# Kernel optimization log

Hardware: AMD Instinct MI355X
Metric: run time of the kernel (lower is better)

Reference implementation:

```python
import jax, jax.numpy as jnp
import numpy as np

N_NODES = 20000
N_EDGES = 320000
N_FEAT = 128
MLP_HID = 64
N_GRAPHS = 16
N_LAYERS = 5
EPS = 1e-5


def setup_inputs() -> dict:
    key = jax.random.key(0)
    ks = jax.random.split(key, 8)
    x = jax.random.normal(ks[0], (N_NODES, N_FEAT), dtype=jnp.float32)
    edge_index = jax.random.randint(ks[1], (2, N_EDGES), 0, N_NODES, dtype=jnp.int64)
    batch = jnp.sort(jax.random.randint(ks[2], (N_NODES,), 0, N_GRAPHS, dtype=jnp.int64))
    W1 = jax.random.normal(ks[3], (N_LAYERS, N_FEAT, MLP_HID), dtype=jnp.float32) * 0.05
    b1 = jnp.zeros((N_LAYERS, MLP_HID), dtype=jnp.float32)
    W2 = jax.random.normal(ks[4], (N_LAYERS, MLP_HID, N_FEAT), dtype=jnp.float32) * 0.05
    b2 = jnp.zeros((N_LAYERS, N_FEAT), dtype=jnp.float32)
    gn_weight = jnp.ones((N_LAYERS, N_FEAT), dtype=jnp.float32)
    gn_bias = jnp.zeros((N_LAYERS, N_FEAT), dtype=jnp.float32)
    gn_scale = jnp.ones((N_LAYERS, N_FEAT), dtype=jnp.float32)
    lin_w = jax.random.normal(ks[5], (N_FEAT, 1), dtype=jnp.float32) * 0.05
    lin_b = jnp.zeros((1,), dtype=jnp.float32)
    return {"x": x, "edge_index": edge_index, "batch": batch,
            "W1": W1, "b1": b1, "W2": W2, "b2": b2,
            "gn_weight": gn_weight, "gn_bias": gn_bias, "gn_scale": gn_scale,
            "lin_w": lin_w, "lin_b": lin_b}


def _conv(h, src, dst, W1, b1, W2, b2):
    # message MLP is per-source-node, so compute MLP(x) once per node,
    # then gather by src and scatter-add to dst. Self loops add m[i] at i.
    m = jax.nn.relu(h @ W1 + b1) @ W2 + b2  # [N, C]
    return jax.ops.segment_sum(m[src], dst, num_segments=N_NODES) + m


def _graph_norm(h, batch, cnt, w, b, a):
    mean = jax.ops.segment_sum(h, batch, num_segments=N_GRAPHS) / cnt  # [G, C]
    out = h - a * mean[batch]
    var = jax.ops.segment_sum(out * out, batch, num_segments=N_GRAPHS) / cnt
    out = out * jax.lax.rsqrt(var[batch] + EPS)
    return w * out + b


def reference(x, edge_index, batch, W1, b1, W2, b2, gn_weight, gn_bias, gn_scale, lin_w, lin_b):
    src, dst = edge_index[0], edge_index[1]
    cnt = jax.ops.segment_sum(jnp.ones((N_NODES, 1), x.dtype), batch,
                              num_segments=N_GRAPHS)
    cnt = jnp.maximum(cnt, 1.0)  # [G, 1]
    h = x
    for i in range(N_LAYERS):
        g = _conv(h, src, dst, W1[i], b1[i], W2[i], b2[i])
        g = _graph_norm(g, batch, cnt, gn_weight[i], gn_bias[i], gn_scale[i])
        g = jax.nn.relu(g)  # dropout is identity in eval mode
        h = g if i == 0 else g + h  # residual from layer 2 onward
    pooled = jax.ops.segment_sum(h, batch, num_segments=N_GRAPHS) / cnt  # [G, C]
    return pooled @ lin_w + lin_b  # [G, 1]
```

## Files before the change

kernel.cpp:

```cpp
#include <hip/hip_runtime.h>

#define N_NODES 20000
#define N_EDGES 320000
#define N_FEAT 128
#define MLP_HID 64
#define N_GRAPHS 16
#define N_LAYERS 5
#define EPS 1e-5f

typedef __attribute__((ext_vector_type(8))) short short8;
typedef __attribute__((ext_vector_type(4))) float f32x4;

__device__ inline float bf2f(unsigned short u) { return __uint_as_float(((unsigned)u) << 16); }
__device__ inline unsigned short f2bf(float f) {
  unsigned u = __float_as_uint(f);
  u += 0x7FFF + ((u >> 16) & 1);
  return (unsigned short)(u >> 16);
}


__global__ __launch_bounds__(256) void k_deg(const int* __restrict__ dst, int* __restrict__ deg) {
  int e = blockIdx.x * 256 + threadIdx.x;
  atomicAdd(&deg[dst[e]], 1);
}

__global__ __launch_bounds__(1024) void k_scan(const int* __restrict__ deg, int* __restrict__ rowptr,
                                               int* __restrict__ cursor, const int* __restrict__ batch,
                                               float* __restrict__ cntf, float* __restrict__ zero_region) {
  __shared__ int sdata[1024];
  __shared__ int spos[17];
  constexpr int CH = 20;
  int t = threadIdx.x;
  for (int i = t; i < 22528; i += 1024) zero_region[i] = 0.0f;
  int base = t * CH;
  int loc[CH];
  int partial = 0;
#pragma unroll
  for (int i = 0; i < CH; i++) {
    int idx = base + i;
    int v = (idx < N_NODES) ? deg[idx] : 0;
    loc[i] = v;
    partial += v;
  }
  sdata[t] = partial;
  __syncthreads();
  for (int off = 1; off < 1024; off <<= 1) {
    int v = (t >= off) ? sdata[t - off] : 0;
    __syncthreads();
    sdata[t] += v;
    __syncthreads();
  }
  int run = sdata[t] - partial;
#pragma unroll
  for (int i = 0; i < CH; i++) {
    int idx = base + i;
    if (idx < N_NODES) {
      rowptr[idx] = run;
      cursor[idx] = run;
      run += loc[i];
    }
  }
  if (t == 1023) rowptr[N_NODES] = sdata[1023];
  if (t < 17) {
    int lo = 0, hi = N_NODES;
    while (lo < hi) {
      int mid = (lo + hi) >> 1;
      if (batch[mid] < t) lo = mid + 1; else hi = mid;
    }
    spos[t] = lo;
  }
  __syncthreads();
  if (t < N_GRAPHS) cntf[t] = fmaxf((float)(spos[t + 1] - spos[t]), 1.0f);
}

__global__ __launch_bounds__(256) void k_fill(const int* __restrict__ src, const int* __restrict__ dst,
                                              int* __restrict__ cursor, int* __restrict__ src_sorted) {
  int e = blockIdx.x * 256 + threadIdx.x;
  int d = dst[e];
  int p = atomicAdd(&cursor[d], 1);
  src_sorted[p] = src[e];
}


__global__ __launch_bounds__(256) void k_prep(const float* __restrict__ W1, const float* __restrict__ W2,
                                              unsigned short* __restrict__ w1t, unsigned short* __restrict__ w2t) {
  int idx = blockIdx.x * 256 + threadIdx.x;
  if (idx < 40960) {
    int l = idx >> 13, rem = idx & 8191;
    int n = rem >> 7, k = rem & 127;
    w1t[idx] = f2bf(W1[l * 8192 + k * 64 + n]);
  } else {
    int j = idx - 40960;
    int l = j >> 13, rem = j & 8191;
    int n = rem >> 6, k = rem & 63;
    w2t[j] = f2bf(W2[l * 8192 + k * 128 + n]);
  }
}


#define PADK 136
#define PADH 72

__global__ __launch_bounds__(256) void k_mlpA(const float* __restrict__ xin, const float* __restrict__ gin,
                                              float* __restrict__ h, unsigned short* __restrict__ mout,
                                              const unsigned short* __restrict__ w1t,
                                              const unsigned short* __restrict__ w2t,
                                              const float* __restrict__ b1, const float* __restrict__ b2,
                                              const int* __restrict__ batch,
                                              const float* __restrict__ s1, const float* __restrict__ s2,
                                              const float* __restrict__ cntf,
                                              const float* __restrict__ gw, const float* __restrict__ gb,
                                              const float* __restrict__ ga, int mode) {
  __shared__ __align__(16) short hS[64 * PADK];
  __shared__ __align__(16) short w1S[64 * PADK];
  __shared__ __align__(16) short hidS[64 * PADH];
  __shared__ __align__(16) short w2S[128 * PADH];
  __shared__ float b1S[64];
  __shared__ float b2S[128];
  int t = threadIdx.x;
  int r0 = blockIdx.x * 64;
#pragma unroll
  for (int i = 0; i < 8; i++) {
    int idx = t + i * 256;
    int row = idx >> 5, c4 = idx & 31;
    int grow = r0 + row;
    float4 v = make_float4(0.f, 0.f, 0.f, 0.f);
    if (grow < N_NODES) {
      if (mode == 0) {
        v = ((const float4*)xin)[(size_t)grow * 32 + c4];
      } else {
        int gg = batch[grow];
        float invc = 1.0f / cntf[gg];
        float4 sm = ((const float4*)s1)[gg * 32 + c4];
        float4 se = ((const float4*)s2)[gg * 32 + c4];
        float4 av = ((const float4*)ga)[c4];
        float4 wv = ((const float4*)gw)[c4];
        float4 bv = ((const float4*)gb)[c4];
        float4 gv = ((const float4*)gin)[(size_t)grow * 32 + c4];
        float4 hv = make_float4(0.f, 0.f, 0.f, 0.f);
        if (mode == 2) hv = ((const float4*)h)[(size_t)grow * 32 + c4];
#define APPLY1(X)                                                         \
        {                                                                 \
          float mean = sm.X * invc;                                       \
          float ex2 = se.X * invc;                                        \
          float ac = av.X;                                                \
          float var = fmaxf(ex2 - mean * mean * (2.0f * ac - ac * ac), 0.0f); \
          float d = gv.X - ac * mean;                                     \
          float y = wv.X * (d * rsqrtf(var + EPS)) + bv.X;                \
          y = fmaxf(y, 0.0f);                                             \
          v.X = y + hv.X;                                                 \
        }
        APPLY1(x) APPLY1(y) APPLY1(z) APPLY1(w)
#undef APPLY1
        ((float4*)h)[(size_t)grow * 32 + c4] = v;
      }
    }
    ushort4 s;
    s.x = f2bf(v.x); s.y = f2bf(v.y); s.z = f2bf(v.z); s.w = f2bf(v.w);
    *(ushort4*)&hS[row * PADK + c4 * 4] = s;
  }
#pragma unroll
  for (int i = 0; i < 4; i++) {
    int idx = t + i * 256;
    *(int4*)&w1S[(idx >> 4) * PADK + (idx & 15) * 8] = ((const int4*)w1t)[idx];
    *(int4*)&w2S[(idx >> 3) * PADH + (idx & 7) * 8] = ((const int4*)w2t)[idx];
  }
  if (t < 64) b1S[t] = b1[t];
  else if (t < 192) b2S[t - 64] = b2[t - 64];
  __syncthreads();

  int w = t >> 6, lane = t & 63, lm = lane & 15, quad = lane >> 4;
  int mrow = w * 16 + lm;
  int orow = w * 16 + quad * 4;

  f32x4 zero = {0.f, 0.f, 0.f, 0.f};
  f32x4 acc[4] = {zero, zero, zero, zero};
#pragma unroll
  for (int k0 = 0; k0 < 128; k0 += 32) {
    short8 a = *(const short8*)&hS[mrow * PADK + k0 + quad * 8];
#pragma unroll
    for (int nt = 0; nt < 4; nt++) {
      short8 b = *(const short8*)&w1S[(nt * 16 + lm) * PADK + k0 + quad * 8];
      acc[nt] = __builtin_amdgcn_mfma_f32_16x16x32_bf16(a, b, acc[nt], 0, 0, 0);
    }
  }
#pragma unroll
  for (int nt = 0; nt < 4; nt++) {
    int col = nt * 16 + lm;
    float bb = b1S[col];
#pragma unroll
    for (int r = 0; r < 4; r++)
      hidS[(orow + r) * PADH + col] = (short)f2bf(fmaxf(acc[nt][r] + bb, 0.0f));
  }
  __syncthreads();

  f32x4 acc2[8] = {zero, zero, zero, zero, zero, zero, zero, zero};
#pragma unroll
  for (int k0 = 0; k0 < 64; k0 += 32) {
    short8 a = *(const short8*)&hidS[mrow * PADH + k0 + quad * 8];
#pragma unroll
    for (int nt = 0; nt < 8; nt++) {
      short8 b = *(const short8*)&w2S[(nt * 16 + lm) * PADH + k0 + quad * 8];
      acc2[nt] = __builtin_amdgcn_mfma_f32_16x16x32_bf16(a, b, acc2[nt], 0, 0, 0);
    }
  }
#pragma unroll
  for (int nt = 0; nt < 8; nt++) {
    int col = nt * 16 + lm;
    float bb = b2S[col];
#pragma unroll
    for (int r = 0; r < 4; r++)
      hS[(orow + r) * PADK + col] = (short)f2bf(acc2[nt][r] + bb);
  }
  __syncthreads();
#pragma unroll
  for (int i = 0; i < 4; i++) {
    int idx = t + i * 256;
    int row = idx >> 4, cc = idx & 15;
    if (r0 + row < N_NODES)
      ((int4*)mout)[(size_t)(r0 + row) * 16 + cc] = *(const int4*)&hS[row * PADK + cc * 8];
  }
}


__global__ __launch_bounds__(256) void k_scatter(const unsigned short* __restrict__ mbf, float* __restrict__ g,
                                                 const int* __restrict__ rowptr, const int* __restrict__ srcs) {
  int node = (blockIdx.x * 256 + threadIdx.x) >> 6;
  int lane = threadIdx.x & 63;
  int quarter = lane >> 4;
  int q16 = lane & 15;
  const float4* m4 = (const float4*)mbf;
  float acc[8];
  union BU { float4 f; unsigned short u[8]; };
  if (quarter == 0) {
    BU U; U.f = m4[(size_t)node * 16 + q16];
#pragma unroll
    for (int j = 0; j < 8; j++) acc[j] = bf2f(U.u[j]);
  } else {
#pragma unroll
    for (int j = 0; j < 8; j++) acc[j] = 0.0f;
  }
  int e = rowptr[node], e1 = rowptr[node + 1];
  for (; e + 16 <= e1; e += 16) {
    int i0 = srcs[e + quarter];
    int i1 = srcs[e + 4 + quarter];
    int i2 = srcs[e + 8 + quarter];
    int i3 = srcs[e + 12 + quarter];
    BU U0, U1, U2, U3;
    U0.f = m4[(size_t)i0 * 16 + q16];
    U1.f = m4[(size_t)i1 * 16 + q16];
    U2.f = m4[(size_t)i2 * 16 + q16];
    U3.f = m4[(size_t)i3 * 16 + q16];
#pragma unroll
    for (int j = 0; j < 8; j++)
      acc[j] += (bf2f(U0.u[j]) + bf2f(U1.u[j])) + (bf2f(U2.u[j]) + bf2f(U3.u[j]));
  }
  for (; e + 4 <= e1; e += 4) {
    BU U0; U0.f = m4[(size_t)srcs[e + quarter] * 16 + q16];
#pragma unroll
    for (int j = 0; j < 8; j++) acc[j] += bf2f(U0.u[j]);
  }
  if (e + quarter < e1) {
    BU U0; U0.f = m4[(size_t)srcs[e + quarter] * 16 + q16];
#pragma unroll
    for (int j = 0; j < 8; j++) acc[j] += bf2f(U0.u[j]);
  }
#pragma unroll
  for (int j = 0; j < 8; j++) {
    acc[j] += __shfl_xor(acc[j], 16);
    acc[j] += __shfl_xor(acc[j], 32);
  }
  if (quarter == 0) {
    float4* g4 = (float4*)(g + (size_t)node * 128 + q16 * 8);
    g4[0] = make_float4(acc[0], acc[1], acc[2], acc[3]);
    g4[1] = make_float4(acc[4], acc[5], acc[6], acc[7]);
  }
}


#define STAT_CHUNK 8

__global__ __launch_bounds__(128) void k_stats(const float* __restrict__ in, const int* __restrict__ batch,
                                               float* __restrict__ s1, float* __restrict__ s2) {
  int n0 = blockIdx.x * STAT_CHUNK;
  int c = threadIdx.x;
  int curg = batch[n0];
  float a1 = 0.0f, a2 = 0.0f;
#pragma unroll
  for (int k = 0; k < STAT_CHUNK; k++) {
    int n = n0 + k;
    int gg = batch[n];
    if (gg != curg) {
      atomicAdd(&s1[curg * 128 + c], a1);
      atomicAdd(&s2[curg * 128 + c], a2);
      a1 = 0.0f; a2 = 0.0f;
      curg = gg;
    }
    float v = in[(size_t)n * 128 + c];
    a1 += v;
    a2 += v * v;
  }
  atomicAdd(&s1[curg * 128 + c], a1);
  atomicAdd(&s2[curg * 128 + c], a2);
}


__global__ __launch_bounds__(256) void k_applyPool(const float* __restrict__ gin, const float* __restrict__ h,
                                                   const int* __restrict__ batch,
                                                   const float* __restrict__ s1, const float* __restrict__ s2,
                                                   const float* __restrict__ cntf,
                                                   const float* __restrict__ gw, const float* __restrict__ gb,
                                                   const float* __restrict__ ga, float* __restrict__ pooled) {
  __shared__ float poolL[128];
  int t = threadIdx.x;
  if (t < 128) poolL[t] = 0.0f;
  __syncthreads();
  int idx = blockIdx.x * 256 + t;
  int n = idx >> 5, c4 = idx & 31;
  int g0 = batch[blockIdx.x * 8];
  int gg = batch[n];
  float invc = 1.0f / cntf[gg];
  float4 sm = ((const float4*)s1)[gg * 32 + c4];
  float4 se = ((const float4*)s2)[gg * 32 + c4];
  float4 av = ((const float4*)ga)[c4];
  float4 wv = ((const float4*)gw)[c4];
  float4 bv = ((const float4*)gb)[c4];
  float4 gv = ((const float4*)gin)[idx];
  float4 hv = ((const float4*)h)[idx];
  float4 o;
#define APPLY1(X)                                                          \
  {                                                                        \
    float mean = sm.X * invc;                                              \
    float ex2 = se.X * invc;                                               \
    float ac = av.X;                                                       \
    float var = fmaxf(ex2 - mean * mean * (2.0f * ac - ac * ac), 0.0f);    \
    float d = gv.X - ac * mean;                                            \
    float y = wv.X * (d * rsqrtf(var + EPS)) + bv.X;                       \
    o.X = fmaxf(y, 0.0f) + hv.X;                                           \
  }
  APPLY1(x) APPLY1(y) APPLY1(z) APPLY1(w)
#undef APPLY1
  if (gg == g0) {
    atomicAdd(&poolL[c4 * 4 + 0], o.x);
    atomicAdd(&poolL[c4 * 4 + 1], o.y);
    atomicAdd(&poolL[c4 * 4 + 2], o.z);
    atomicAdd(&poolL[c4 * 4 + 3], o.w);
  } else {
    atomicAdd(&pooled[gg * 128 + c4 * 4 + 0], o.x);
    atomicAdd(&pooled[gg * 128 + c4 * 4 + 1], o.y);
    atomicAdd(&pooled[gg * 128 + c4 * 4 + 2], o.z);
    atomicAdd(&pooled[gg * 128 + c4 * 4 + 3], o.w);
  }
  __syncthreads();
  if (t < 128) atomicAdd(&pooled[g0 * 128 + t], poolL[t]);
}


__global__ __launch_bounds__(256) void k_final(const float* __restrict__ pooled, const float* __restrict__ cntf,
                                               const float* __restrict__ lw, const float* __restrict__ lb,
                                               float* __restrict__ out) {
  int lane = threadIdx.x & 63, wave = threadIdx.x >> 6;
  for (int gi = 0; gi < 4; gi++) {
    int gidx = wave * 4 + gi;
    float s = pooled[gidx * 128 + lane] * lw[lane] + pooled[gidx * 128 + 64 + lane] * lw[64 + lane];
    for (int o = 32; o >= 1; o >>= 1) s += __shfl_down(s, o);
    if (lane == 0) out[gidx] = s / cntf[gidx] + lb[0];
  }
}


extern "C" void kernel_launch(void* const* d_in, const int* in_sizes, int n_in,
                              void* d_out, int out_size, void* d_ws, size_t ws_size,
                              hipStream_t stream) {
  const float* x = (const float*)d_in[0];
  const int* ei = (const int*)d_in[1];
  const int* batch = (const int*)d_in[2];
  const float* W1 = (const float*)d_in[3];
  const float* b1 = (const float*)d_in[4];
  const float* W2 = (const float*)d_in[5];
  const float* b2 = (const float*)d_in[6];
  const float* gnw = (const float*)d_in[7];
  const float* gnb = (const float*)d_in[8];
  const float* gna = (const float*)d_in[9];
  const float* lw = (const float*)d_in[10];
  const float* lb = (const float*)d_in[11];
  float* out = (float*)d_out;

  const int* srcI = ei;
  const int* dstI = ei + N_EDGES;

  char* p = (char*)d_ws;
  float* hbuf = (float*)(p + 0);
  unsigned short* mbuf = (unsigned short*)(p + 10240000);
  float* gbuf = (float*)(p + 15360000);
  int* src_sorted = (int*)(p + 25600000);
  int* rowptr = (int*)(p + 26880000);
  int* cursor = (int*)(p + 26960128);
  int* deg = (int*)(p + 27040256);
  float* cntf = (float*)(p + 27120384);
  unsigned short* w1t = (unsigned short*)(p + 27120512);
  unsigned short* w2t = (unsigned short*)(p + 27202432);
  float* sbufs = (float*)(p + 27284352);
  float* pooled = (float*)(p + 27366272);

  hipMemsetAsync(deg, 0, N_NODES * sizeof(int), stream);
  k_deg<<<N_EDGES / 256, 256, 0, stream>>>(dstI, deg);
  k_scan<<<1, 1024, 0, stream>>>(deg, rowptr, cursor, batch, cntf, sbufs);
  k_fill<<<N_EDGES / 256, 256, 0, stream>>>(srcI, dstI, cursor, src_sorted);
  k_prep<<<320, 256, 0, stream>>>(W1, W2, w1t, w2t);

  for (int i = 0; i < N_LAYERS; i++) {
    int pi = (i > 0) ? (i - 1) : 0;
    int mode = (i == 0) ? 0 : (i == 1 ? 1 : 2);
    k_mlpA<<<(N_NODES + 63) / 64, 256, 0, stream>>>(
        x, gbuf, hbuf, mbuf, w1t + (size_t)i * 8192, w2t + (size_t)i * 8192,
        b1 + (size_t)i * 64, b2 + (size_t)i * 128,
        batch, sbufs + (size_t)pi * 4096, sbufs + (size_t)pi * 4096 + 2048, cntf,
        gnw + (size_t)pi * 128, gnb + (size_t)pi * 128, gna + (size_t)pi * 128, mode);
    k_scatter<<<N_NODES / 4, 256, 0, stream>>>(mbuf, gbuf, rowptr, src_sorted);
    k_stats<<<N_NODES / STAT_CHUNK, 128, 0, stream>>>(gbuf, batch,
                                                      sbufs + (size_t)i * 4096, sbufs + (size_t)i * 4096 + 2048);
  }

  k_applyPool<<<N_NODES * N_FEAT / 4 / 256, 256, 0, stream>>>(
      gbuf, hbuf, batch, sbufs + 4 * 4096, sbufs + 4 * 4096 + 2048, cntf,
      gnw + 4 * 128, gnb + 4 * 128, gna + 4 * 128, pooled);
  k_final<<<1, 256, 0, stream>>>(pooled, cntf, lw, lb, out);
}
```

Before: 349.4 us.

## Fuse per-layer kernels into one cooperative persistent kernel with grid syncs

Replaces the per-layer sequence of MLP, gather-scatter, stats, apply-pool and final kernels with a single cooperative kernel. The kernel loops over layers, runs each stage as a grid-stride loop over tiles or tasks, and separates stages with grid.sync(). This removes about 17 kernel launches and their launch gaps. In exchange the grid is capped by occupancy, which limits parallelism in the memory-bound gather stage. Grid-wide barriers add their own cost, and the tile loop reloads the weights into shared memory for every tile.

```diff
diff --git a/kernel.cpp b/kernel.cpp
--- a/kernel.cpp
+++ b/kernel.cpp
@@ -1,4 +1,7 @@
 #include <hip/hip_runtime.h>
+#include <hip/hip_cooperative_groups.h>
+
+namespace cg = cooperative_groups;
 
 #define N_NODES 20000
 #define N_EDGES 320000
@@ -80,7 +83,6 @@
   int p = atomicAdd(&cursor[d], 1);
   src_sorted[p] = src[e];
 }
-
 
 __global__ __launch_bounds__(256) void k_prep(const float* __restrict__ W1, const float* __restrict__ W2,
                                               unsigned short* __restrict__ w1t, unsigned short* __restrict__ w2t) {
@@ -100,271 +102,302 @@
 
 #define PADK 136
 #define PADH 72
-
-__global__ __launch_bounds__(256) void k_mlpA(const float* __restrict__ xin, const float* __restrict__ gin,
-                                              float* __restrict__ h, unsigned short* __restrict__ mout,
-                                              const unsigned short* __restrict__ w1t,
-                                              const unsigned short* __restrict__ w2t,
-                                              const float* __restrict__ b1, const float* __restrict__ b2,
-                                              const int* __restrict__ batch,
-                                              const float* __restrict__ s1, const float* __restrict__ s2,
-                                              const float* __restrict__ cntf,
-                                              const float* __restrict__ gw, const float* __restrict__ gb,
-                                              const float* __restrict__ ga, int mode) {
-  __shared__ __align__(16) short hS[64 * PADK];
-  __shared__ __align__(16) short w1S[64 * PADK];
-  __shared__ __align__(16) short hidS[64 * PADH];
-  __shared__ __align__(16) short w2S[128 * PADH];
-  __shared__ float b1S[64];
-  __shared__ float b2S[128];
+#define SMEM_BYTES 63232
+
+__global__ __launch_bounds__(256, 2) void k_mega(
+    const float* __restrict__ x, const int* __restrict__ batch,
+    const float* __restrict__ b1g, const float* __restrict__ b2g,
+    const float* __restrict__ gnw, const float* __restrict__ gnb, const float* __restrict__ gna,
+    const float* __restrict__ lw, const float* __restrict__ lb,
+    float* __restrict__ h, unsigned short* __restrict__ m, float* __restrict__ g,
+    const int* __restrict__ rowptr, const int* __restrict__ srcs,
+    const float* __restrict__ cntf, const unsigned short* __restrict__ w1t,
+    const unsigned short* __restrict__ w2t,
+    float* __restrict__ sbufs, float* __restrict__ pooled, float* __restrict__ out) {
+  cg::grid_group grid = cg::this_grid();
+  __shared__ __align__(16) char smem[SMEM_BYTES];
+  short* hS = (short*)(smem);
+  short* w1S = (short*)(smem + 17408);
+  short* hidS = (short*)(smem + 34816);
+  short* w2S = (short*)(smem + 44032);
+  float* b1S = (float*)(smem + 62464);
+  float* b2S = (float*)(smem + 62720);
   int t = threadIdx.x;
-  int r0 = blockIdx.x * 64;
-#pragma unroll
-  for (int i = 0; i < 8; i++) {
-    int idx = t + i * 256;
-    int row = idx >> 5, c4 = idx & 31;
-    int grow = r0 + row;
-    float4 v = make_float4(0.f, 0.f, 0.f, 0.f);
-    if (grow < N_NODES) {
-      if (mode == 0) {
-        v = ((const float4*)xin)[(size_t)grow * 32 + c4];
+
+  for (int layer = 0; layer < N_LAYERS; layer++) {
+    const unsigned short* w1 = w1t + (size_t)layer * 8192;
+    const unsigned short* w2 = w2t + (size_t)layer * 8192;
+    const float* b1 = b1g + (size_t)layer * 64;
+    const float* b2 = b2g + (size_t)layer * 128;
+    int pi = (layer > 0) ? (layer - 1) : 0;
+    const float* s1 = sbufs + (size_t)pi * 4096;
+    const float* s2 = s1 + 2048;
+    const float* gw = gnw + (size_t)pi * 128;
+    const float* gb = gnb + (size_t)pi * 128;
+    const float* ga = gna + (size_t)pi * 128;
+    int mode = (layer == 0) ? 0 : (layer == 1 ? 1 : 2);
+
+    for (int tile = blockIdx.x; tile < 313; tile += gridDim.x) {
+      int r0 = tile * 64;
+#pragma unroll
+      for (int i = 0; i < 8; i++) {
+        int idx = t + i * 256;
+        int row = idx >> 5, c4 = idx & 31;
+        int grow = r0 + row;
+        float4 v = make_float4(0.f, 0.f, 0.f, 0.f);
+        if (grow < N_NODES) {
+          if (mode == 0) {
+            v = ((const float4*)x)[(size_t)grow * 32 + c4];
+          } else {
+            int gg = batch[grow];
+            float invc = 1.0f / cntf[gg];
+            float4 sm = ((const float4*)s1)[gg * 32 + c4];
+            float4 se = ((const float4*)s2)[gg * 32 + c4];
+            float4 av = ((const float4*)ga)[c4];
+            float4 wv = ((const float4*)gw)[c4];
+            float4 bv = ((const float4*)gb)[c4];
+            float4 gv = ((const float4*)g)[(size_t)grow * 32 + c4];
+            float4 hv = make_float4(0.f, 0.f, 0.f, 0.f);
+            if (mode == 2) hv = ((const float4*)h)[(size_t)grow * 32 + c4];
+#define APPLY1(X)                                                         \
+            {                                                             \
+              float mean = sm.X * invc;                                   \
+              float ex2 = se.X * invc;                                    \
+              float ac = av.X;                                            \
+              float var = fmaxf(ex2 - mean * mean * (2.0f * ac - ac * ac), 0.0f); \
+              float d = gv.X - ac * mean;                                 \
+              float y = wv.X * (d * rsqrtf(var + EPS)) + bv.X;            \
+              y = fmaxf(y, 0.0f);                                         \
+              v.X = y + hv.X;                                             \
+            }
+            APPLY1(x) APPLY1(y) APPLY1(z) APPLY1(w)
+#undef APPLY1
+            ((float4*)h)[(size_t)grow * 32 + c4] = v;
+          }
+        }
+        ushort4 s;
+        s.x = f2bf(v.x); s.y = f2bf(v.y); s.z = f2bf(v.z); s.w = f2bf(v.w);
+        *(ushort4*)&hS[row * PADK + c4 * 4] = s;
+      }
+#pragma unroll
+      for (int i = 0; i < 4; i++) {
+        int idx = t + i * 256;
+        *(int4*)&w1S[(idx >> 4) * PADK + (idx & 15) * 8] = ((const int4*)w1)[idx];
+        *(int4*)&w2S[(idx >> 3) * PADH + (idx & 7) * 8] = ((const int4*)w2)[idx];
+      }
+      if (t < 64) b1S[t] = b1[t];
+      else if (t < 192) b2S[t - 64] = b2[t - 64];
+      __syncthreads();
+
+      int w = t >> 6, lane = t & 63, lm = lane & 15, quad = lane >> 4;
+      int mrow = w * 16 + lm;
+      int orow = w * 16 + quad * 4;
+
+      f32x4 zero = {0.f, 0.f, 0.f, 0.f};
+      f32x4 acc[4] = {zero, zero, zero, zero};
+#pragma unroll
+      for (int k0 = 0; k0 < 128; k0 += 32) {
+        short8 a = *(const short8*)&hS[mrow * PADK + k0 + quad * 8];
+#pragma unroll
+        for (int nt = 0; nt < 4; nt++) {
+          short8 b = *(const short8*)&w1S[(nt * 16 + lm) * PADK + k0 + quad * 8];
+          acc[nt] = __builtin_amdgcn_mfma_f32_16x16x32_bf16(a, b, acc[nt], 0, 0, 0);
+        }
+      }
+#pragma unroll
+      for (int nt = 0; nt < 4; nt++) {
+        int col = nt * 16 + lm;
+        float bb = b1S[col];
+#pragma unroll
+        for (int r = 0; r < 4; r++)
+          hidS[(orow + r) * PADH + col] = (short)f2bf(fmaxf(acc[nt][r] + bb, 0.0f));
+      }
+      __syncthreads();
+
+      f32x4 acc2[8] = {zero, zero, zero, zero, zero, zero, zero, zero};
+#pragma unroll
+      for (int k0 = 0; k0 < 64; k0 += 32) {
+        short8 a = *(const short8*)&hidS[mrow * PADH + k0 + quad * 8];
+#pragma unroll
+        for (int nt = 0; nt < 8; nt++) {
+          short8 b = *(const short8*)&w2S[(nt * 16 + lm) * PADH + k0 + quad * 8];
+          acc2[nt] = __builtin_amdgcn_mfma_f32_16x16x32_bf16(a, b, acc2[nt], 0, 0, 0);
+        }
+      }
+#pragma unroll
+      for (int nt = 0; nt < 8; nt++) {
+        int col = nt * 16 + lm;
+        float bb = b2S[col];
+#pragma unroll
+        for (int r = 0; r < 4; r++)
+          hS[(orow + r) * PADK + col] = (short)f2bf(acc2[nt][r] + bb);
+      }
+      __syncthreads();
+#pragma unroll
+      for (int i = 0; i < 4; i++) {
+        int idx = t + i * 256;
+        int row = idx >> 4, cc = idx & 15;
+        if (r0 + row < N_NODES)
+          ((int4*)m)[(size_t)(r0 + row) * 16 + cc] = *(const int4*)&hS[row * PADK + cc * 8];
+      }
+      __syncthreads();
+    }
+    grid.sync();
+
+    {
+      int lane = t & 63;
+      int quarter = lane >> 4;
+      int q16 = lane & 15;
+      const float4* m4 = (const float4*)m;
+      for (int task = blockIdx.x; task < 5000; task += gridDim.x) {
+        int node = task * 4 + (t >> 6);
+        float acc[8];
+        union BU { float4 f; unsigned short u[8]; };
+        if (quarter == 0) {
+          BU U; U.f = m4[(size_t)node * 16 + q16];
+#pragma unroll
+          for (int j = 0; j < 8; j++) acc[j] = bf2f(U.u[j]);
+        } else {
+#pragma unroll
+          for (int j = 0; j < 8; j++) acc[j] = 0.0f;
+        }
+        int e = rowptr[node], e1 = rowptr[node + 1];
+        for (; e + 16 <= e1; e += 16) {
+          int i0 = srcs[e + quarter];
+          int i1 = srcs[e + 4 + quarter];
+          int i2 = srcs[e + 8 + quarter];
+          int i3 = srcs[e + 12 + quarter];
+          BU U0, U1, U2, U3;
+          U0.f = m4[(size_t)i0 * 16 + q16];
+          U1.f = m4[(size_t)i1 * 16 + q16];
+          U2.f = m4[(size_t)i2 * 16 + q16];
+          U3.f = m4[(size_t)i3 * 16 + q16];
+#pragma unroll
+          for (int j = 0; j < 8; j++)
+            acc[j] += (bf2f(U0.u[j]) + bf2f(U1.u[j])) + (bf2f(U2.u[j]) + bf2f(U3.u[j]));
+        }
+        for (; e + 4 <= e1; e += 4) {
+          BU U0; U0.f = m4[(size_t)srcs[e + quarter] * 16 + q16];
+#pragma unroll
+          for (int j = 0; j < 8; j++) acc[j] += bf2f(U0.u[j]);
+        }
+        if (e + quarter < e1) {
+          BU U0; U0.f = m4[(size_t)srcs[e + quarter] * 16 + q16];
+#pragma unroll
+          for (int j = 0; j < 8; j++) acc[j] += bf2f(U0.u[j]);
+        }
+#pragma unroll
+        for (int j = 0; j < 8; j++) {
+          acc[j] += __shfl_xor(acc[j], 16);
+          acc[j] += __shfl_xor(acc[j], 32);
+        }
+        if (quarter == 0) {
+          float4* g4 = (float4*)(g + (size_t)node * 128 + q16 * 8);
+          g4[0] = make_float4(acc[0], acc[1], acc[2], acc[3]);
+          g4[1] = make_float4(acc[4], acc[5], acc[6], acc[7]);
+        }
+      }
+    }
+    grid.sync();
+
+    {
+      float* s1w = sbufs + (size_t)layer * 4096;
+      float* s2w = s1w + 2048;
+      int half = t >> 7, c = t & 127;
+      for (int task = blockIdx.x; task < 1250; task += gridDim.x) {
+        int n0 = task * 16 + half * 8;
+        int curg = batch[n0];
+        float a1 = 0.0f, a2 = 0.0f;
+#pragma unroll
+        for (int k = 0; k < 8; k++) {
+          int n = n0 + k;
+          int gg = batch[n];
+          if (gg != curg) {
+            atomicAdd(&s1w[curg * 128 + c], a1);
+            atomicAdd(&s2w[curg * 128 + c], a2);
+            a1 = 0.0f; a2 = 0.0f;
+            curg = gg;
+          }
+          float v = g[(size_t)n * 128 + c];
+          a1 += v;
+          a2 += v * v;
+        }
+        atomicAdd(&s1w[curg * 128 + c], a1);
+        atomicAdd(&s2w[curg * 128 + c], a2);
+      }
+    }
+    grid.sync();
+  }
+
+  {
+    const float* s1 = sbufs + 4 * 4096;
+    const float* s2 = s1 + 2048;
+    const float* gw = gnw + 4 * 128;
+    const float* gb = gnb + 4 * 128;
+    const float* ga = gna + 4 * 128;
+    float4* poolT = (float4*)smem;
+    int c4 = t & 31;
+    for (int task = blockIdx.x; task < 2500; task += gridDim.x) {
+      int idx = task * 256 + t;
+      int n = idx >> 5;
+      int gg = batch[n];
+      float invc = 1.0f / cntf[gg];
+      float4 sm = ((const float4*)s1)[gg * 32 + c4];
+      float4 se = ((const float4*)s2)[gg * 32 + c4];
+      float4 av = ((const float4*)ga)[c4];
+      float4 wv = ((const float4*)gw)[c4];
+      float4 bv = ((const float4*)gb)[c4];
+      float4 gv = ((const float4*)g)[idx];
+      float4 hv = ((const float4*)h)[idx];
+      float4 o;
+#define APPLY1(X)                                                          \
+      {                                                                    \
+        float mean = sm.X * invc;                                          \
+        float ex2 = se.X * invc;                                           \
+        float ac = av.X;                                                   \
+        float var = fmaxf(ex2 - mean * mean * (2.0f * ac - ac * ac), 0.0f);\
+        float d = gv.X - ac * mean;                                        \
+        float y = wv.X * (d * rsqrtf(var + EPS)) + bv.X;                   \
+        o.X = fmaxf(y, 0.0f) + hv.X;                                       \
+      }
+      APPLY1(x) APPLY1(y) APPLY1(z) APPLY1(w)
+#undef APPLY1
+      poolT[t] = o;
+      __syncthreads();
+      int n0 = task * 8;
+      if (batch[n0] == batch[n0 + 7]) {
+        if (t < 32) {
+          float4 s = poolT[t];
+#pragma unroll
+          for (int r = 1; r < 8; r++) {
+            float4 v = poolT[r * 32 + t];
+            s.x += v.x; s.y += v.y; s.z += v.z; s.w += v.w;
+          }
+          int gt = batch[n0];
+          atomicAdd(&pooled[gt * 128 + t * 4 + 0], s.x);
+          atomicAdd(&pooled[gt * 128 + t * 4 + 1], s.y);
+          atomicAdd(&pooled[gt * 128 + t * 4 + 2], s.z);
+          atomicAdd(&pooled[gt * 128 + t * 4 + 3], s.w);
+        }
       } else {
-        int gg = batch[grow];
-        float invc = 1.0f / cntf[gg];
-        float4 sm = ((const float4*)s1)[gg * 32 + c4];
-        float4 se = ((const float4*)s2)[gg * 32 + c4];
-        float4 av = ((const float4*)ga)[c4];
-        float4 wv = ((const float4*)gw)[c4];
-        float4 bv = ((const float4*)gb)[c4];
-        float4 gv = ((const float4*)gin)[(size_t)grow * 32 + c4];
-        float4 hv = make_float4(0.f, 0.f, 0.f, 0.f);
-        if (mode == 2) hv = ((const float4*)h)[(size_t)grow * 32 + c4];
-#define APPLY1(X)                                                         \
-        {                                                                 \
-          float mean = sm.X * invc;                                       \
-          float ex2 = se.X * invc;                                        \
-          float ac = av.X;                                                \
-          float var = fmaxf(ex2 - mean * mean * (2.0f * ac - ac * ac), 0.0f); \
-          float d = gv.X - ac * mean;                                     \
-          float y = wv.X * (d * rsqrtf(var + EPS)) + bv.X;                \
-          y = fmaxf(y, 0.0f);                                             \
-          v.X = y + hv.X;                                                 \
-        }
-        APPLY1(x) APPLY1(y) APPLY1(z) APPLY1(w)
-#undef APPLY1
-        ((float4*)h)[(size_t)grow * 32 + c4] = v;
-      }
-    }
-    ushort4 s;
-    s.x = f2bf(v.x); s.y = f2bf(v.y); s.z = f2bf(v.z); s.w = f2bf(v.w);
-    *(ushort4*)&hS[row * PADK + c4 * 4] = s;
-  }
-#pragma unroll
-  for (int i = 0; i < 4; i++) {
-    int idx = t + i * 256;
-    *(int4*)&w1S[(idx >> 4) * PADK + (idx & 15) * 8] = ((const int4*)w1t)[idx];
-    *(int4*)&w2S[(idx >> 3) * PADH + (idx & 7) * 8] = ((const int4*)w2t)[idx];
-  }
-  if (t < 64) b1S[t] = b1[t];
-  else if (t < 192) b2S[t - 64] = b2[t - 64];
-  __syncthreads();
-
-  int w = t >> 6, lane = t & 63, lm = lane & 15, quad = lane >> 4;
-  int mrow = w * 16 + lm;
-  int orow = w * 16 + quad * 4;
-
-  f32x4 zero = {0.f, 0.f, 0.f, 0.f};
-  f32x4 acc[4] = {zero, zero, zero, zero};
-#pragma unroll
-  for (int k0 = 0; k0 < 128; k0 += 32) {
-    short8 a = *(const short8*)&hS[mrow * PADK + k0 + quad * 8];
-#pragma unroll
-    for (int nt = 0; nt < 4; nt++) {
-      short8 b = *(const short8*)&w1S[(nt * 16 + lm) * PADK + k0 + quad * 8];
-      acc[nt] = __builtin_amdgcn_mfma_f32_16x16x32_bf16(a, b, acc[nt], 0, 0, 0);
-    }
-  }
-#pragma unroll
-  for (int nt = 0; nt < 4; nt++) {
-    int col = nt * 16 + lm;
-    float bb = b1S[col];
-#pragma unroll
-    for (int r = 0; r < 4; r++)
-      hidS[(orow + r) * PADH + col] = (short)f2bf(fmaxf(acc[nt][r] + bb, 0.0f));
-  }
-  __syncthreads();
-
-  f32x4 acc2[8] = {zero, zero, zero, zero, zero, zero, zero, zero};
-#pragma unroll
-  for (int k0 = 0; k0 < 64; k0 += 32) {
-    short8 a = *(const short8*)&hidS[mrow * PADH + k0 + quad * 8];
-#pragma unroll
-    for (int nt = 0; nt < 8; nt++) {
-      short8 b = *(const short8*)&w2S[(nt * 16 + lm) * PADH + k0 + quad * 8];
-      acc2[nt] = __builtin_amdgcn_mfma_f32_16x16x32_bf16(a, b, acc2[nt], 0, 0, 0);
-    }
-  }
-#pragma unroll
-  for (int nt = 0; nt < 8; nt++) {
-    int col = nt * 16 + lm;
-    float bb = b2S[col];
-#pragma unroll
-    for (int r = 0; r < 4; r++)
-      hS[(orow + r) * PADK + col] = (short)f2bf(acc2[nt][r] + bb);
-  }
-  __syncthreads();
-#pragma unroll
-  for (int i = 0; i < 4; i++) {
-    int idx = t + i * 256;
-    int row = idx >> 4, cc = idx & 15;
-    if (r0 + row < N_NODES)
-      ((int4*)mout)[(size_t)(r0 + row) * 16 + cc] = *(const int4*)&hS[row * PADK + cc * 8];
-  }
-}
-
-
-__global__ __launch_bounds__(256) void k_scatter(const unsigned short* __restrict__ mbf, float* __restrict__ g,
-                                                 const int* __restrict__ rowptr, const int* __restrict__ srcs) {
-  int node = (blockIdx.x * 256 + threadIdx.x) >> 6;
-  int lane = threadIdx.x & 63;
-  int quarter = lane >> 4;
-  int q16 = lane & 15;
-  const float4* m4 = (const float4*)mbf;
-  float acc[8];
-  union BU { float4 f; unsigned short u[8]; };
-  if (quarter == 0) {
-    BU U; U.f = m4[(size_t)node * 16 + q16];
-#pragma unroll
-    for (int j = 0; j < 8; j++) acc[j] = bf2f(U.u[j]);
-  } else {
-#pragma unroll
-    for (int j = 0; j < 8; j++) acc[j] = 0.0f;
-  }
-  int e = rowptr[node], e1 = rowptr[node + 1];
-  for (; e + 16 <= e1; e += 16) {
-    int i0 = srcs[e + quarter];
-    int i1 = srcs[e + 4 + quarter];
-    int i2 = srcs[e + 8 + quarter];
-    int i3 = srcs[e + 12 + quarter];
-    BU U0, U1, U2, U3;
-    U0.f = m4[(size_t)i0 * 16 + q16];
-    U1.f = m4[(size_t)i1 * 16 + q16];
-    U2.f = m4[(size_t)i2 * 16 + q16];
-    U3.f = m4[(size_t)i3 * 16 + q16];
-#pragma unroll
-    for (int j = 0; j < 8; j++)
-      acc[j] += (bf2f(U0.u[j]) + bf2f(U1.u[j])) + (bf2f(U2.u[j]) + bf2f(U3.u[j]));
-  }
-  for (; e + 4 <= e1; e += 4) {
-    BU U0; U0.f = m4[(size_t)srcs[e + quarter] * 16 + q16];
-#pragma unroll
-    for (int j = 0; j < 8; j++) acc[j] += bf2f(U0.u[j]);
-  }
-  if (e + quarter < e1) {
-    BU U0; U0.f = m4[(size_t)srcs[e + quarter] * 16 + q16];
-#pragma unroll
-    for (int j = 0; j < 8; j++) acc[j] += bf2f(U0.u[j]);
-  }
-#pragma unroll
-  for (int j = 0; j < 8; j++) {
-    acc[j] += __shfl_xor(acc[j], 16);
-    acc[j] += __shfl_xor(acc[j], 32);
-  }
-  if (quarter == 0) {
-    float4* g4 = (float4*)(g + (size_t)node * 128 + q16 * 8);
-    g4[0] = make_float4(acc[0], acc[1], acc[2], acc[3]);
-    g4[1] = make_float4(acc[4], acc[5], acc[6], acc[7]);
-  }
-}
-
-
-#define STAT_CHUNK 8
-
-__global__ __launch_bounds__(128) void k_stats(const float* __restrict__ in, const int* __restrict__ batch,
-                                               float* __restrict__ s1, float* __restrict__ s2) {
-  int n0 = blockIdx.x * STAT_CHUNK;
-  int c = threadIdx.x;
-  int curg = batch[n0];
-  float a1 = 0.0f, a2 = 0.0f;
-#pragma unroll
-  for (int k = 0; k < STAT_CHUNK; k++) {
-    int n = n0 + k;
-    int gg = batch[n];
-    if (gg != curg) {
-      atomicAdd(&s1[curg * 128 + c], a1);
-      atomicAdd(&s2[curg * 128 + c], a2);
-      a1 = 0.0f; a2 = 0.0f;
-      curg = gg;
-    }
-    float v = in[(size_t)n * 128 + c];
-    a1 += v;
-    a2 += v * v;
-  }
-  atomicAdd(&s1[curg * 128 + c], a1);
-  atomicAdd(&s2[curg * 128 + c], a2);
-}
-
-
-__global__ __launch_bounds__(256) void k_applyPool(const float* __restrict__ gin, const float* __restrict__ h,
-                                                   const int* __restrict__ batch,
-                                                   const float* __restrict__ s1, const float* __restrict__ s2,
-                                                   const float* __restrict__ cntf,
-                                                   const float* __restrict__ gw, const float* __restrict__ gb,
-                                                   const float* __restrict__ ga, float* __restrict__ pooled) {
-  __shared__ float poolL[128];
-  int t = threadIdx.x;
-  if (t < 128) poolL[t] = 0.0f;
-  __syncthreads();
-  int idx = blockIdx.x * 256 + t;
-  int n = idx >> 5, c4 = idx & 31;
-  int g0 = batch[blockIdx.x * 8];
-  int gg = batch[n];
-  float invc = 1.0f / cntf[gg];
-  float4 sm = ((const float4*)s1)[gg * 32 + c4];
-  float4 se = ((const float4*)s2)[gg * 32 + c4];
-  float4 av = ((const float4*)ga)[c4];
-  float4 wv = ((const float4*)gw)[c4];
-  float4 bv = ((const float4*)gb)[c4];
-  float4 gv = ((const float4*)gin)[idx];
-  float4 hv = ((const float4*)h)[idx];
-  float4 o;
-#define APPLY1(X)                                                          \
-  {                                                                        \
-    float mean = sm.X * invc;                                              \
-    float ex2 = se.X * invc;                                               \
-    float ac = av.X;                                                       \
-    float var = fmaxf(ex2 - mean * mean * (2.0f * ac - ac * ac), 0.0f);    \
-    float d = gv.X - ac * mean;                                            \
-    float y = wv.X * (d * rsqrtf(var + EPS)) + bv.X;                       \
-    o.X = fmaxf(y, 0.0f) + hv.X;                                           \
-  }
-  APPLY1(x) APPLY1(y) APPLY1(z) APPLY1(w)
-#undef APPLY1
-  if (gg == g0) {
-    atomicAdd(&poolL[c4 * 4 + 0], o.x);
-    atomicAdd(&poolL[c4 * 4 + 1], o.y);
-    atomicAdd(&poolL[c4 * 4 + 2], o.z);
-    atomicAdd(&poolL[c4 * 4 + 3], o.w);
-  } else {
-    atomicAdd(&pooled[gg * 128 + c4 * 4 + 0], o.x);
-    atomicAdd(&pooled[gg * 128 + c4 * 4 + 1], o.y);
-    atomicAdd(&pooled[gg * 128 + c4 * 4 + 2], o.z);
-    atomicAdd(&pooled[gg * 128 + c4 * 4 + 3], o.w);
-  }
-  __syncthreads();
-  if (t < 128) atomicAdd(&pooled[g0 * 128 + t], poolL[t]);
-}
-
-
-__global__ __launch_bounds__(256) void k_final(const float* __restrict__ pooled, const float* __restrict__ cntf,
-                                               const float* __restrict__ lw, const float* __restrict__ lb,
-                                               float* __restrict__ out) {
-  int lane = threadIdx.x & 63, wave = threadIdx.x >> 6;
-  for (int gi = 0; gi < 4; gi++) {
-    int gidx = wave * 4 + gi;
-    float s = pooled[gidx * 128 + lane] * lw[lane] + pooled[gidx * 128 + 64 + lane] * lw[64 + lane];
-    for (int o = 32; o >= 1; o >>= 1) s += __shfl_down(s, o);
-    if (lane == 0) out[gidx] = s / cntf[gidx] + lb[0];
+        atomicAdd(&pooled[gg * 128 + c4 * 4 + 0], o.x);
+        atomicAdd(&pooled[gg * 128 + c4 * 4 + 1], o.y);
+        atomicAdd(&pooled[gg * 128 + c4 * 4 + 2], o.z);
+        atomicAdd(&pooled[gg * 128 + c4 * 4 + 3], o.w);
+      }
+      __syncthreads();
+    }
+  }
+  grid.sync();
+
+  if (blockIdx.x == 0) {
+    int lane = t & 63, wave = t >> 6;
+    for (int gi = 0; gi < 4; gi++) {
+      int gidx = wave * 4 + gi;
+      float s = pooled[gidx * 128 + lane] * lw[lane] + pooled[gidx * 128 + 64 + lane] * lw[64 + lane];
+      for (int o = 32; o >= 1; o >>= 1) s += __shfl_down(s, o);
+      if (lane == 0) out[gidx] = s / cntf[gidx] + lb[0];
+    }
   }
 }
 
@@ -409,21 +442,17 @@
   k_fill<<<N_EDGES / 256, 256, 0, stream>>>(srcI, dstI, cursor, src_sorted);
   k_prep<<<320, 256, 0, stream>>>(W1, W2, w1t, w2t);
 
-  for (int i = 0; i < N_LAYERS; i++) {
-    int pi = (i > 0) ? (i - 1) : 0;
-    int mode = (i == 0) ? 0 : (i == 1 ? 1 : 2);
-    k_mlpA<<<(N_NODES + 63) / 64, 256, 0, stream>>>(
-        x, gbuf, hbuf, mbuf, w1t + (size_t)i * 8192, w2t + (size_t)i * 8192,
-        b1 + (size_t)i * 64, b2 + (size_t)i * 128,
-        batch, sbufs + (size_t)pi * 4096, sbufs + (size_t)pi * 4096 + 2048, cntf,
-        gnw + (size_t)pi * 128, gnb + (size_t)pi * 128, gna + (size_t)pi * 128, mode);
-    k_scatter<<<N_NODES / 4, 256, 0, stream>>>(mbuf, gbuf, rowptr, src_sorted);
-    k_stats<<<N_NODES / STAT_CHUNK, 128, 0, stream>>>(gbuf, batch,
-                                                      sbufs + (size_t)i * 4096, sbufs + (size_t)i * 4096 + 2048);
-  }
-
-  k_applyPool<<<N_NODES * N_FEAT / 4 / 256, 256, 0, stream>>>(
-      gbuf, hbuf, batch, sbufs + 4 * 4096, sbufs + 4 * 4096 + 2048, cntf,
-      gnw + 4 * 128, gnb + 4 * 128, gna + 4 * 128, pooled);
-  k_final<<<1, 256, 0, stream>>>(pooled, cntf, lw, lb, out);
-}
+  int maxPerCU = 0;
+  hipOccupancyMaxActiveBlocksPerMultiprocessor(&maxPerCU, k_mega, 256, 0);
+  int nblk = maxPerCU * 256;
+  if (nblk > 512) nblk = 512;
+  if (nblk < 64) nblk = 64;
+
+  void* args[] = {
+      (void*)&x, (void*)&batch, (void*)&b1, (void*)&b2,
+      (void*)&gnw, (void*)&gnb, (void*)&gna, (void*)&lw, (void*)&lb,
+      (void*)&hbuf, (void*)&mbuf, (void*)&gbuf,
+      (void*)&rowptr, (void*)&src_sorted, (void*)&cntf,
+      (void*)&w1t, (void*)&w2t, (void*)&sbufs, (void*)&pooled, (void*)&out};
+  hipLaunchCooperativeKernel(k_mega, dim3(nblk), dim3(256), args, 0, stream);
+}
```

New measurement: 1.073 ms. 3.07x slower.
